# Optimization experiments

Hardware: AMD Instinct MI355X
Metric: run time of the kernel (lower is better)

Reference implementation:

```python
import jax, jax.numpy as jnp
import numpy as np

L, E, D, R, B = 3, 4, 1024, 64, 32768

def setup_inputs() -> dict:
    key = jax.random.key(0)
    ks = jax.random.split(key, 6)
    sU = (2.0 / (D + R)) ** 0.5  # xavier_normal std for [E, D, R]
    sC = (2.0 / (R + R)) ** 0.5
    sG = (2.0 / (D + 1)) ** 0.5
    return {
        "inputs": jax.random.normal(ks[0], (B, D), jnp.float32),
        "U": jax.random.normal(ks[1], (L, E, D, R), jnp.float32) * sU,
        "V": jax.random.normal(ks[2], (L, E, D, R), jnp.float32) * sU,
        "C": jax.random.normal(ks[3], (L, E, R, R), jnp.float32) * sC,
        "gating_w": jax.random.normal(ks[4], (E, D), jnp.float32) * sG,
        "bias": jnp.zeros((L, D), jnp.float32),
    }

def reference(inputs, U, V, C, gating_w, bias):
    x0 = inputs            # [B, D]
    x_l = inputs           # [B, D]
    for i in range(L):
        # per-expert gating scores on current x_l, softmax over experts
        gate = jax.nn.softmax(jnp.einsum("bd,ed->be", x_l, gating_w), axis=1)  # [B, E]
        # low-rank cross: V^T x -> tanh -> C v -> tanh -> U v
        v = jnp.tanh(jnp.einsum("bd,edr->ber", x_l, V[i]))     # [B, E, R]
        v = jnp.tanh(jnp.einsum("ers,bes->ber", C[i], v))      # [B, E, R]
        uv = jnp.einsum("edr,ber->bed", U[i], v)               # [B, E, D]
        dot = x0[:, None, :] * (uv + bias[i][None, None, :])   # [B, E, D]
        moe = jnp.einsum("bed,be->bd", dot, gate)              # [B, D]
        x_l = moe + x_l
    return x_l
```

## Files before the change

kernel.cpp:

```cpp
#include <hip/hip_runtime.h>
#include <hip/hip_bf16.h>

typedef __bf16 bf16_t;
typedef bf16_t bf16x8 __attribute__((ext_vector_type(8)));
typedef float f32x4 __attribute__((ext_vector_type(4)));

#define L_NUM 3
#define E_NUM 4
#define D_DIM 1024
#define R_DIM 64
#define B_ROWS 32768
#define BT 32
#define TPB 512
#define N1 272
#define XL_STRIDE 1032
#define T1_STRIDE 264

#define VT_ELEMS (L_NUM * N1 * D_DIM)
#define UT_ELEMS (L_NUM * D_DIM * 256)
#define CB_ELEMS (L_NUM * E_NUM * R_DIM * R_DIM)

#define MFMA16(a, b, c) __builtin_amdgcn_mfma_f32_16x16x32_bf16((a), (b), (c), 0, 0, 0)

__device__ __forceinline__ ushort f2b(float f) {
  union { float f; unsigned u; } x; x.f = f;
  unsigned r = (x.u + 0x7fffu + ((x.u >> 16) & 1u)) >> 16;
  return (ushort)r;
}
__device__ __forceinline__ float b2f(ushort h) {
  union { unsigned u; float f; } x; x.u = ((unsigned)h) << 16;
  return x.f;
}
__device__ __forceinline__ float tanh_fast(float x) {
  float cx = fminf(fmaxf(x, -15.f), 15.f);
  float e = __expf(2.f * cx);
  return (e - 1.f) / (e + 1.f);
}


__global__ void pack_vt_kernel(const float* __restrict__ V, const float* __restrict__ gw,
                               ushort* __restrict__ vt) {
  int idx = blockIdx.x * 256 + threadIdx.x;
  if (idx >= VT_ELEMS) return;
  int d = idx & (D_DIM - 1);
  int n = (idx >> 10) % N1;
  int l = idx / (N1 * D_DIM);
  float val = 0.f;
  if (n < 256) {
    int e = n >> 6, r = n & 63;
    val = V[(((l * E_NUM + e) * D_DIM) + d) * R_DIM + r];
  } else if (n < 260) {
    val = gw[(n - 256) * D_DIM + d];
  }
  vt[idx] = f2b(val);
}

__global__ void pack_ut_kernel(const float* __restrict__ U, ushort* __restrict__ ut) {
  int idx = blockIdx.x * 256 + threadIdx.x;
  if (idx >= UT_ELEMS) return;
  int er = idx & 255;
  int d = (idx >> 8) & (D_DIM - 1);
  int l = idx >> 18;
  int e = er >> 6, r = er & 63;
  ut[idx] = f2b(U[((l * E_NUM + e) * D_DIM + d) * R_DIM + r]);
}

__global__ void pack_cb_kernel(const float* __restrict__ C, ushort* __restrict__ cb) {
  int idx = blockIdx.x * 256 + threadIdx.x;
  if (idx >= CB_ELEMS) return;
  cb[idx] = f2b(C[idx]);
}


__global__ __launch_bounds__(TPB, 2) void crossnet_fused(
    const float* __restrict__ inputs, const float* __restrict__ bias,
    const ushort* __restrict__ Vt, const ushort* __restrict__ Ut,
    const ushort* __restrict__ Cb, float* __restrict__ out) {
  __shared__ ushort xl[BT * XL_STRIDE];
  __shared__ ushort x0s[BT * XL_STRIDE];
  __shared__ ushort t1[BT * T1_STRIDE];
  __shared__ float glog[BT * 4];
  __shared__ float gate[BT * 4];

  const int tid = threadIdx.x;
  const int wave = tid >> 6;
  const int lane = tid & 63;
  const int l15 = lane & 15;
  const int quad = lane >> 4;
  const long rowbase = (long)blockIdx.x * BT;

  #pragma unroll
  for (int i = 0; i < 16; ++i) {
    int idx = tid + i * TPB;
    int r = idx >> 8;
    int c4 = idx & 255;
    float4 v = ((const float4*)(inputs + (rowbase + r) * D_DIM))[c4];
    ushort4 h;
    h.x = f2b(v.x); h.y = f2b(v.y); h.z = f2b(v.z); h.w = f2b(v.w);
    *(ushort4*)&xl[r * XL_STRIDE + c4 * 4] = h;
    *(ushort4*)&x0s[r * XL_STRIDE + c4 * 4] = h;
  }

  float xlr[8][2][4];
  #pragma unroll
  for (int nt = 0; nt < 8; ++nt)
    #pragma unroll
    for (int m = 0; m < 2; ++m)
      #pragma unroll
      for (int rg = 0; rg < 4; ++rg) {
        int row = m * 16 + quad * 4 + rg;
        int col = wave * 128 + nt * 16 + l15;
        xlr[nt][m][rg] = inputs[(rowbase + row) * D_DIM + col];
      }
  __syncthreads();

  const f32x4 zf = {0.f, 0.f, 0.f, 0.f};

  for (int l = 0; l < L_NUM; ++l) {
    const ushort* vtl = Vt + l * N1 * D_DIM;
    const ushort* utl = Ut + l * D_DIM * 256;
    const ushort* cbl = Cb + l * E_NUM * R_DIM * R_DIM;

    f32x4 acc1[3][2];
    #pragma unroll
    for (int t = 0; t < 3; ++t) { acc1[t][0] = zf; acc1[t][1] = zf; }

    const ushort* xa0 = &xl[l15 * XL_STRIDE + quad * 8];
    const ushort* xa1 = &xl[(16 + l15) * XL_STRIDE + quad * 8];
    const ushort* vb0 = vtl + (wave * 32 + l15) * D_DIM + quad * 8;
    const ushort* vb1 = vb0 + 16 * D_DIM;
    if (wave == 7) {
      const ushort* vb2 = vtl + (256 + l15) * D_DIM + quad * 8;
      #pragma unroll 4
      for (int k0 = 0; k0 < D_DIM; k0 += 32) {
        bf16x8 a0 = *(const bf16x8*)(xa0 + k0);
        bf16x8 a1 = *(const bf16x8*)(xa1 + k0);
        bf16x8 b0 = *(const bf16x8*)(vb0 + k0);
        bf16x8 b1 = *(const bf16x8*)(vb1 + k0);
        bf16x8 b2 = *(const bf16x8*)(vb2 + k0);
        acc1[0][0] = MFMA16(a0, b0, acc1[0][0]);
        acc1[0][1] = MFMA16(a1, b0, acc1[0][1]);
        acc1[1][0] = MFMA16(a0, b1, acc1[1][0]);
        acc1[1][1] = MFMA16(a1, b1, acc1[1][1]);
        acc1[2][0] = MFMA16(a0, b2, acc1[2][0]);
        acc1[2][1] = MFMA16(a1, b2, acc1[2][1]);
      }
    } else {
      #pragma unroll 4
      for (int k0 = 0; k0 < D_DIM; k0 += 32) {
        bf16x8 a0 = *(const bf16x8*)(xa0 + k0);
        bf16x8 a1 = *(const bf16x8*)(xa1 + k0);
        bf16x8 b0 = *(const bf16x8*)(vb0 + k0);
        bf16x8 b1 = *(const bf16x8*)(vb1 + k0);
        acc1[0][0] = MFMA16(a0, b0, acc1[0][0]);
        acc1[0][1] = MFMA16(a1, b0, acc1[0][1]);
        acc1[1][0] = MFMA16(a0, b1, acc1[1][0]);
        acc1[1][1] = MFMA16(a1, b1, acc1[1][1]);
      }
    }

    #pragma unroll
    for (int t = 0; t < 2; ++t) {
      int ncol = wave * 32 + t * 16 + l15;
      #pragma unroll
      for (int m = 0; m < 2; ++m)
        #pragma unroll
        for (int rg = 0; rg < 4; ++rg) {
          int row = m * 16 + quad * 4 + rg;
          t1[row * T1_STRIDE + ncol] = f2b(tanh_fast(acc1[t][m][rg]));
        }
    }
    if (wave == 7 && l15 < 4) {
      #pragma unroll
      for (int m = 0; m < 2; ++m)
        #pragma unroll
        for (int rg = 0; rg < 4; ++rg)
          glog[(m * 16 + quad * 4 + rg) * 4 + l15] = acc1[2][m][rg];
    }
    __syncthreads();

    if (tid < BT) {
      float g0 = glog[tid * 4 + 0], g1 = glog[tid * 4 + 1];
      float g2 = glog[tid * 4 + 2], g3 = glog[tid * 4 + 3];
      float mx = fmaxf(fmaxf(g0, g1), fmaxf(g2, g3));
      float e0 = __expf(g0 - mx), e1 = __expf(g1 - mx);
      float e2 = __expf(g2 - mx), e3 = __expf(g3 - mx);
      float inv = 1.f / (e0 + e1 + e2 + e3);
      gate[tid * 4 + 0] = e0 * inv; gate[tid * 4 + 1] = e1 * inv;
      gate[tid * 4 + 2] = e2 * inv; gate[tid * 4 + 3] = e3 * inv;
    }

    const int e = wave >> 1;
    const int nh = wave & 1;
    f32x4 acc2[2][2];
    acc2[0][0] = zf; acc2[0][1] = zf; acc2[1][0] = zf; acc2[1][1] = zf;
    #pragma unroll
    for (int k0 = 0; k0 < 64; k0 += 32) {
      bf16x8 a0 = *(const bf16x8*)&t1[l15 * T1_STRIDE + e * 64 + k0 + quad * 8];
      bf16x8 a1 = *(const bf16x8*)&t1[(16 + l15) * T1_STRIDE + e * 64 + k0 + quad * 8];
      bf16x8 b0 = *(const bf16x8*)&cbl[(e * 64 + nh * 32 + l15) * 64 + k0 + quad * 8];
      bf16x8 b1 = *(const bf16x8*)&cbl[(e * 64 + nh * 32 + 16 + l15) * 64 + k0 + quad * 8];
      acc2[0][0] = MFMA16(a0, b0, acc2[0][0]);
      acc2[0][1] = MFMA16(a1, b0, acc2[0][1]);
      acc2[1][0] = MFMA16(a0, b1, acc2[1][0]);
      acc2[1][1] = MFMA16(a1, b1, acc2[1][1]);
    }
    __syncthreads();
    #pragma unroll
    for (int t = 0; t < 2; ++t) {
      int ncol = e * 64 + nh * 32 + t * 16 + l15;
      #pragma unroll
      for (int m = 0; m < 2; ++m)
        #pragma unroll
        for (int rg = 0; rg < 4; ++rg) {
          int row = m * 16 + quad * 4 + rg;
          float g = gate[row * 4 + e];
          t1[row * T1_STRIDE + ncol] = f2b(g * tanh_fast(acc2[t][m][rg]));
        }
    }
    __syncthreads();

    f32x4 acc3[8][2];
    #pragma unroll
    for (int nt = 0; nt < 8; ++nt) { acc3[nt][0] = zf; acc3[nt][1] = zf; }
    const ushort* wa0 = &t1[l15 * T1_STRIDE + quad * 8];
    const ushort* wa1 = &t1[(16 + l15) * T1_STRIDE + quad * 8];
    const ushort* ub = utl + (wave * 128 + l15) * 256 + quad * 8;
    #pragma unroll 2
    for (int k0 = 0; k0 < 256; k0 += 32) {
      bf16x8 a0 = *(const bf16x8*)(wa0 + k0);
      bf16x8 a1 = *(const bf16x8*)(wa1 + k0);
      #pragma unroll
      for (int nt = 0; nt < 8; ++nt) {
        bf16x8 b = *(const bf16x8*)(ub + nt * 16 * 256 + k0);
        acc3[nt][0] = MFMA16(a0, b, acc3[nt][0]);
        acc3[nt][1] = MFMA16(a1, b, acc3[nt][1]);
      }
    }

    #pragma unroll
    for (int nt = 0; nt < 8; ++nt) {
      int col = wave * 128 + nt * 16 + l15;
      float bv = bias[l * D_DIM + col];
      #pragma unroll
      for (int m = 0; m < 2; ++m)
        #pragma unroll
        for (int rg = 0; rg < 4; ++rg) {
          int row = m * 16 + quad * 4 + rg;
          float x0v = b2f(x0s[row * XL_STRIDE + col]);
          float xn = xlr[nt][m][rg] + x0v * (acc3[nt][m][rg] + bv);
          xlr[nt][m][rg] = xn;
          xl[row * XL_STRIDE + col] = f2b(xn);
        }
    }
    __syncthreads();
  }

  #pragma unroll
  for (int nt = 0; nt < 8; ++nt) {
    int col = wave * 128 + nt * 16 + l15;
    #pragma unroll
    for (int m = 0; m < 2; ++m)
      #pragma unroll
      for (int rg = 0; rg < 4; ++rg) {
        int row = m * 16 + quad * 4 + rg;
        out[(rowbase + row) * D_DIM + col] = xlr[nt][m][rg];
      }
  }
}

extern "C" void kernel_launch(void* const* d_in, const int* in_sizes, int n_in,
                              void* d_out, int out_size, void* d_ws, size_t ws_size,
                              hipStream_t stream) {
  (void)in_sizes; (void)n_in; (void)out_size; (void)ws_size;
  const float* inputs = (const float*)d_in[0];
  const float* U      = (const float*)d_in[1];
  const float* V      = (const float*)d_in[2];
  const float* C      = (const float*)d_in[3];
  const float* gw     = (const float*)d_in[4];
  const float* bias   = (const float*)d_in[5];
  float* out = (float*)d_out;

  ushort* vt = (ushort*)d_ws;
  ushort* ut = vt + VT_ELEMS;
  ushort* cb = ut + UT_ELEMS;

  pack_vt_kernel<<<(VT_ELEMS + 255) / 256, 256, 0, stream>>>(V, gw, vt);
  pack_ut_kernel<<<(UT_ELEMS + 255) / 256, 256, 0, stream>>>(U, ut);
  pack_cb_kernel<<<(CB_ELEMS + 255) / 256, 256, 0, stream>>>(C, cb);

  crossnet_fused<<<B_ROWS / BT, TPB, 0, stream>>>(inputs, bias, vt, ut, cb, out);
}
```

Measured before the change: 686.1 us.

## Halve rows per block and compute gating softmax per wave via shuffles

```diff
diff --git a/kernel.cpp b/kernel.cpp
--- a/kernel.cpp
+++ b/kernel.cpp
@@ -10,7 +10,7 @@
 #define D_DIM 1024
 #define R_DIM 64
 #define B_ROWS 32768
-#define BT 32
+#define BT 16
 #define TPB 512
 #define N1 272
 #define XL_STRIDE 1032
@@ -72,15 +72,13 @@
 }
 
 
-__global__ __launch_bounds__(TPB, 2) void crossnet_fused(
+__global__ __launch_bounds__(TPB, 4) void crossnet_fused(
     const float* __restrict__ inputs, const float* __restrict__ bias,
     const ushort* __restrict__ Vt, const ushort* __restrict__ Ut,
     const ushort* __restrict__ Cb, float* __restrict__ out) {
   __shared__ ushort xl[BT * XL_STRIDE];
   __shared__ ushort x0s[BT * XL_STRIDE];
   __shared__ ushort t1[BT * T1_STRIDE];
-  __shared__ float glog[BT * 4];
-  __shared__ float gate[BT * 4];
 
   const int tid = threadIdx.x;
   const int wave = tid >> 6;
@@ -90,7 +88,7 @@
   const long rowbase = (long)blockIdx.x * BT;
 
   #pragma unroll
-  for (int i = 0; i < 16; ++i) {
+  for (int i = 0; i < 8; ++i) {
     int idx = tid + i * TPB;
     int r = idx >> 8;
     int c4 = idx & 255;
@@ -101,140 +99,104 @@
     *(ushort4*)&x0s[r * XL_STRIDE + c4 * 4] = h;
   }
 
-  float xlr[8][2][4];
+  float xlr[8][4];
   #pragma unroll
   for (int nt = 0; nt < 8; ++nt)
     #pragma unroll
-    for (int m = 0; m < 2; ++m)
-      #pragma unroll
-      for (int rg = 0; rg < 4; ++rg) {
-        int row = m * 16 + quad * 4 + rg;
-        int col = wave * 128 + nt * 16 + l15;
-        xlr[nt][m][rg] = inputs[(rowbase + row) * D_DIM + col];
-      }
+    for (int rg = 0; rg < 4; ++rg) {
+      int row = quad * 4 + rg;
+      int col = wave * 128 + nt * 16 + l15;
+      xlr[nt][rg] = inputs[(rowbase + row) * D_DIM + col];
+    }
   __syncthreads();
 
   const f32x4 zf = {0.f, 0.f, 0.f, 0.f};
+  const int eC = wave >> 1;
+  const int nh = wave & 1;
 
   for (int l = 0; l < L_NUM; ++l) {
     const ushort* vtl = Vt + l * N1 * D_DIM;
     const ushort* utl = Ut + l * D_DIM * 256;
     const ushort* cbl = Cb + l * E_NUM * R_DIM * R_DIM;
 
-    f32x4 acc1[3][2];
-    #pragma unroll
-    for (int t = 0; t < 3; ++t) { acc1[t][0] = zf; acc1[t][1] = zf; }
+    f32x4 acc1[2];
+    acc1[0] = zf; acc1[1] = zf;
+    f32x4 accg = zf;
 
     const ushort* xa0 = &xl[l15 * XL_STRIDE + quad * 8];
-    const ushort* xa1 = &xl[(16 + l15) * XL_STRIDE + quad * 8];
     const ushort* vb0 = vtl + (wave * 32 + l15) * D_DIM + quad * 8;
     const ushort* vb1 = vb0 + 16 * D_DIM;
-    if (wave == 7) {
-      const ushort* vb2 = vtl + (256 + l15) * D_DIM + quad * 8;
-      #pragma unroll 4
-      for (int k0 = 0; k0 < D_DIM; k0 += 32) {
-        bf16x8 a0 = *(const bf16x8*)(xa0 + k0);
-        bf16x8 a1 = *(const bf16x8*)(xa1 + k0);
-        bf16x8 b0 = *(const bf16x8*)(vb0 + k0);
-        bf16x8 b1 = *(const bf16x8*)(vb1 + k0);
-        bf16x8 b2 = *(const bf16x8*)(vb2 + k0);
-        acc1[0][0] = MFMA16(a0, b0, acc1[0][0]);
-        acc1[0][1] = MFMA16(a1, b0, acc1[0][1]);
-        acc1[1][0] = MFMA16(a0, b1, acc1[1][0]);
-        acc1[1][1] = MFMA16(a1, b1, acc1[1][1]);
-        acc1[2][0] = MFMA16(a0, b2, acc1[2][0]);
-        acc1[2][1] = MFMA16(a1, b2, acc1[2][1]);
-      }
-    } else {
-      #pragma unroll 4
-      for (int k0 = 0; k0 < D_DIM; k0 += 32) {
-        bf16x8 a0 = *(const bf16x8*)(xa0 + k0);
-        bf16x8 a1 = *(const bf16x8*)(xa1 + k0);
-        bf16x8 b0 = *(const bf16x8*)(vb0 + k0);
-        bf16x8 b1 = *(const bf16x8*)(vb1 + k0);
-        acc1[0][0] = MFMA16(a0, b0, acc1[0][0]);
-        acc1[0][1] = MFMA16(a1, b0, acc1[0][1]);
-        acc1[1][0] = MFMA16(a0, b1, acc1[1][0]);
-        acc1[1][1] = MFMA16(a1, b1, acc1[1][1]);
-      }
+    const ushort* vbg = vtl + (256 + l15) * D_DIM + quad * 8;
+    #pragma unroll 4
+    for (int k0 = 0; k0 < D_DIM; k0 += 32) {
+      bf16x8 a0 = *(const bf16x8*)(xa0 + k0);
+      bf16x8 b0 = *(const bf16x8*)(vb0 + k0);
+      bf16x8 b1 = *(const bf16x8*)(vb1 + k0);
+      bf16x8 bg = *(const bf16x8*)(vbg + k0);
+      acc1[0] = MFMA16(a0, b0, acc1[0]);
+      acc1[1] = MFMA16(a0, b1, acc1[1]);
+      accg    = MFMA16(a0, bg, accg);
     }
 
     #pragma unroll
     for (int t = 0; t < 2; ++t) {
       int ncol = wave * 32 + t * 16 + l15;
       #pragma unroll
-      for (int m = 0; m < 2; ++m)
-        #pragma unroll
-        for (int rg = 0; rg < 4; ++rg) {
-          int row = m * 16 + quad * 4 + rg;
-          t1[row * T1_STRIDE + ncol] = f2b(tanh_fast(acc1[t][m][rg]));
-        }
-    }
-    if (wave == 7 && l15 < 4) {
-      #pragma unroll
-      for (int m = 0; m < 2; ++m)
-        #pragma unroll
-        for (int rg = 0; rg < 4; ++rg)
-          glog[(m * 16 + quad * 4 + rg) * 4 + l15] = acc1[2][m][rg];
-    }
-    __syncthreads();
-
-    if (tid < BT) {
-      float g0 = glog[tid * 4 + 0], g1 = glog[tid * 4 + 1];
-      float g2 = glog[tid * 4 + 2], g3 = glog[tid * 4 + 3];
-      float mx = fmaxf(fmaxf(g0, g1), fmaxf(g2, g3));
-      float e0 = __expf(g0 - mx), e1 = __expf(g1 - mx);
-      float e2 = __expf(g2 - mx), e3 = __expf(g3 - mx);
-      float inv = 1.f / (e0 + e1 + e2 + e3);
-      gate[tid * 4 + 0] = e0 * inv; gate[tid * 4 + 1] = e1 * inv;
-      gate[tid * 4 + 2] = e2 * inv; gate[tid * 4 + 3] = e3 * inv;
-    }
-
-    const int e = wave >> 1;
-    const int nh = wave & 1;
-    f32x4 acc2[2][2];
-    acc2[0][0] = zf; acc2[0][1] = zf; acc2[1][0] = zf; acc2[1][1] = zf;
+      for (int rg = 0; rg < 4; ++rg)
+        t1[(quad * 4 + rg) * T1_STRIDE + ncol] = f2b(tanh_fast(acc1[t][rg]));
+    }
+
+    float gr[4];
+    {
+      const int qbase = lane & 48;
+      #pragma unroll
+      for (int rg = 0; rg < 4; ++rg) {
+        float g0 = __shfl(accg[rg], qbase + 0);
+        float g1 = __shfl(accg[rg], qbase + 1);
+        float g2 = __shfl(accg[rg], qbase + 2);
+        float g3 = __shfl(accg[rg], qbase + 3);
+        float mx = fmaxf(fmaxf(g0, g1), fmaxf(g2, g3));
+        float e0 = __expf(g0 - mx), e1 = __expf(g1 - mx);
+        float e2 = __expf(g2 - mx), e3 = __expf(g3 - mx);
+        float inv = 1.f / (e0 + e1 + e2 + e3);
+        float ge = (eC == 0) ? e0 : (eC == 1) ? e1 : (eC == 2) ? e2 : e3;
+        gr[rg] = ge * inv;
+      }
+    }
+    __syncthreads();
+
+    f32x4 acc2[2];
+    acc2[0] = zf; acc2[1] = zf;
     #pragma unroll
     for (int k0 = 0; k0 < 64; k0 += 32) {
-      bf16x8 a0 = *(const bf16x8*)&t1[l15 * T1_STRIDE + e * 64 + k0 + quad * 8];
-      bf16x8 a1 = *(const bf16x8*)&t1[(16 + l15) * T1_STRIDE + e * 64 + k0 + quad * 8];
-      bf16x8 b0 = *(const bf16x8*)&cbl[(e * 64 + nh * 32 + l15) * 64 + k0 + quad * 8];
-      bf16x8 b1 = *(const bf16x8*)&cbl[(e * 64 + nh * 32 + 16 + l15) * 64 + k0 + quad * 8];
-      acc2[0][0] = MFMA16(a0, b0, acc2[0][0]);
-      acc2[0][1] = MFMA16(a1, b0, acc2[0][1]);
-      acc2[1][0] = MFMA16(a0, b1, acc2[1][0]);
-      acc2[1][1] = MFMA16(a1, b1, acc2[1][1]);
+      bf16x8 a0 = *(const bf16x8*)&t1[l15 * T1_STRIDE + eC * 64 + k0 + quad * 8];
+      bf16x8 b0 = *(const bf16x8*)&cbl[(eC * 64 + nh * 32 + l15) * 64 + k0 + quad * 8];
+      bf16x8 b1 = *(const bf16x8*)&cbl[(eC * 64 + nh * 32 + 16 + l15) * 64 + k0 + quad * 8];
+      acc2[0] = MFMA16(a0, b0, acc2[0]);
+      acc2[1] = MFMA16(a0, b1, acc2[1]);
     }
     __syncthreads();
     #pragma unroll
     for (int t = 0; t < 2; ++t) {
-      int ncol = e * 64 + nh * 32 + t * 16 + l15;
-      #pragma unroll
-      for (int m = 0; m < 2; ++m)
-        #pragma unroll
-        for (int rg = 0; rg < 4; ++rg) {
-          int row = m * 16 + quad * 4 + rg;
-          float g = gate[row * 4 + e];
-          t1[row * T1_STRIDE + ncol] = f2b(g * tanh_fast(acc2[t][m][rg]));
-        }
-    }
-    __syncthreads();
-
-    f32x4 acc3[8][2];
-    #pragma unroll
-    for (int nt = 0; nt < 8; ++nt) { acc3[nt][0] = zf; acc3[nt][1] = zf; }
+      int ncol = eC * 64 + nh * 32 + t * 16 + l15;
+      #pragma unroll
+      for (int rg = 0; rg < 4; ++rg)
+        t1[(quad * 4 + rg) * T1_STRIDE + ncol] = f2b(gr[rg] * tanh_fast(acc2[t][rg]));
+    }
+    __syncthreads();
+
+    f32x4 acc3[8];
+    #pragma unroll
+    for (int nt = 0; nt < 8; ++nt) acc3[nt] = zf;
     const ushort* wa0 = &t1[l15 * T1_STRIDE + quad * 8];
-    const ushort* wa1 = &t1[(16 + l15) * T1_STRIDE + quad * 8];
     const ushort* ub = utl + (wave * 128 + l15) * 256 + quad * 8;
     #pragma unroll 2
     for (int k0 = 0; k0 < 256; k0 += 32) {
       bf16x8 a0 = *(const bf16x8*)(wa0 + k0);
-      bf16x8 a1 = *(const bf16x8*)(wa1 + k0);
       #pragma unroll
       for (int nt = 0; nt < 8; ++nt) {
         bf16x8 b = *(const bf16x8*)(ub + nt * 16 * 256 + k0);
-        acc3[nt][0] = MFMA16(a0, b, acc3[nt][0]);
-        acc3[nt][1] = MFMA16(a1, b, acc3[nt][1]);
+        acc3[nt] = MFMA16(a0, b, acc3[nt]);
       }
     }
 
@@ -243,15 +205,13 @@
       int col = wave * 128 + nt * 16 + l15;
       float bv = bias[l * D_DIM + col];
       #pragma unroll
-      for (int m = 0; m < 2; ++m)
-        #pragma unroll
-        for (int rg = 0; rg < 4; ++rg) {
-          int row = m * 16 + quad * 4 + rg;
-          float x0v = b2f(x0s[row * XL_STRIDE + col]);
-          float xn = xlr[nt][m][rg] + x0v * (acc3[nt][m][rg] + bv);
-          xlr[nt][m][rg] = xn;
-          xl[row * XL_STRIDE + col] = f2b(xn);
-        }
+      for (int rg = 0; rg < 4; ++rg) {
+        int row = quad * 4 + rg;
+        float x0v = b2f(x0s[row * XL_STRIDE + col]);
+        float xn = xlr[nt][rg] + x0v * (acc3[nt][rg] + bv);
+        xlr[nt][rg] = xn;
+        xl[row * XL_STRIDE + col] = f2b(xn);
+      }
     }
     __syncthreads();
   }
@@ -260,12 +220,10 @@
   for (int nt = 0; nt < 8; ++nt) {
     int col = wave * 128 + nt * 16 + l15;
     #pragma unroll
-    for (int m = 0; m < 2; ++m)
-      #pragma unroll
-      for (int rg = 0; rg < 4; ++rg) {
-        int row = m * 16 + quad * 4 + rg;
-        out[(rowbase + row) * D_DIM + col] = xlr[nt][m][rg];
-      }
+    for (int rg = 0; rg < 4; ++rg) {
+      int row = quad * 4 + rg;
+      out[(rowbase + row) * D_DIM + col] = xlr[nt][rg];
+    }
   }
 }
 
```

Result: slower. 1.098 ms (+60.1%).
